# Kernel tuning notes

Hardware: AMD Instinct MI355X
Metric: run time of the kernel (lower is better)

## Reference

```python
import math
import jax, jax.numpy as jnp
import numpy as np
from jax.scipy.special import xlogy

B, N, INP, E = 128, 16, 1024, 512
MU, CLF, PLCY = 512, 512, 512
M = N - 1          # merges (full tree)
T = N + M          # total tree tokens
L = N + M - 1      # logits matrix side
NOISE_STD, MASK_VAL = 0.01, -9e20
SFTMX_EPS, STD_EPS = 1e-20, 1e-20


def _mlp3(x, w1, b1, w2, b2, w3, b3):
    h = jax.nn.relu(x @ w1 + b1)
    h = jax.nn.relu(h @ w2 + b2)
    return h @ w3 + b3


def _lin(key, fi, fo):
    lim = math.sqrt(6.0 / (fi + fo))  # xavier uniform
    return (jax.random.uniform(key, (fi, fo), minval=-lim, maxval=lim, dtype=jnp.float32),
            jnp.full((fo,), 0.001, dtype=jnp.float32))


def setup_inputs():
    key = jax.random.key(0)
    ks = jax.random.split(key, 16)
    inp = {"x": jax.random.normal(ks[0], (B, N, INP), dtype=jnp.float32)}
    inp["lift_w"], inp["lift_b"] = _lin(ks[1], INP, E)
    inp["unlift_w"], inp["unlift_b"] = _lin(ks[2], E, INP)
    inp["enc_w1"], inp["enc_b1"] = _lin(ks[3], 2 * E, MU)
    inp["enc_w2"], inp["enc_b2"] = _lin(ks[4], MU, MU)
    inp["enc_w3"], inp["enc_b3"] = _lin(ks[5], MU, E)
    inp["dec_w1"], inp["dec_b1"] = _lin(ks[6], E, MU)
    inp["dec_w2"], inp["dec_b2"] = _lin(ks[7], MU, MU)
    inp["dec_w3"], inp["dec_b3"] = _lin(ks[8], MU, 2 * E)
    inp["clf_w1"], inp["clf_b1"] = _lin(ks[9], E, CLF)
    inp["clf_w2"], inp["clf_b2"] = _lin(ks[10], CLF, CLF)
    inp["clf_w3"], inp["clf_b3"] = _lin(ks[11], CLF, 2)
    inp["pol_w1"], inp["pol_b1"] = _lin(ks[12], 2 * E, PLCY)
    inp["pol_w2"], inp["pol_b2"] = _lin(ks[13], PLCY, PLCY)
    inp["pol_w3"], inp["pol_b3"] = _lin(ks[14], PLCY, 1)
    return inp


def _forward(x, lift_w, lift_b, unlift_w, unlift_b,
             enc_w1, enc_b1, enc_w2, enc_b2, enc_w3, enc_b3,
             dec_w1, dec_b1, dec_w2, dec_b2, dec_w3, dec_b3,
             clf_w1, clf_b1, clf_w2, clf_b2, clf_w3, clf_b3,
             pol_w1, pol_b1, pol_w2, pol_b2, pol_w3, pol_b3):
    sg = jax.lax.stop_gradient
    enc = lambda z: _mlp3(z, enc_w1, enc_b1, enc_w2, enc_b2, enc_w3, enc_b3)
    dec = lambda z: _mlp3(z, dec_w1, dec_b1, dec_w2, dec_b2, dec_w3, dec_b3)
    clf = lambda z: _mlp3(z, clf_w1, clf_b1, clf_w2, clf_b2, clf_w3, clf_b3)
    pol = lambda z: _mlp3(z, pol_w1, pol_b1, pol_w2, pol_b2, pol_w3, pol_b3)
    base = jax.random.key(42)
    b_idx = jnp.arange(B)

    # lift + noise
    u = x @ lift_w + lift_b
    u = u + NOISE_STD * jax.random.normal(jax.random.fold_in(base, 7), u.shape, u.dtype)

    logits_mtx = jnp.full((B, L, L), MASK_VAL, dtype=jnp.float32)
    # iter 0: score all ordered pairs (i,j), i != j, among input tokens (vectorized)
    ii, jj = np.where(~np.eye(N, dtype=bool))                 # P = N*(N-1) static pairs
    pair_x = jnp.concatenate([u[:, ii], u[:, jj]], axis=-1)   # [B,P,2E]
    logits_mtx = logits_mtx.at[:, ii, jj].set(pol(sg(pair_x))[..., 0])

    active = jnp.tile(jnp.arange(N, dtype=jnp.int32), (B, 1))
    step_losses = jnp.zeros(B, dtype=jnp.float32)
    entropies = jnp.zeros(B, dtype=jnp.float32)
    actions, log_probs, rewards = [], [], []

    for it in range(M):
        A = active.shape[1]  # = N - it (active-token count at entry)
        if it > 0:
            nt = N + it - 1                      # newest merged token (last in active)
            act = active[:, :-1]                 # [B, A-1] older active tokens
            u_act = u[b_idx[:, None], act]       # [B, A-1, E]
            u_nt = jnp.broadcast_to(u[:, nt][:, None, :], u_act.shape)
            lg_f = pol(sg(jnp.concatenate([u_nt, u_act], -1)))[..., 0]
            lg_b = pol(sg(jnp.concatenate([u_act, u_nt], -1)))[..., 0]
            logits_mtx = logits_mtx.at[b_idx[:, None], nt, act].set(lg_f)
            logits_mtx = logits_mtx.at[b_idx[:, None], act, nt].set(lg_b)

        flat = logits_mtx.reshape(B, L * L)      # temp == 1 for learned policy
        p = jax.nn.softmax(flat, axis=1)
        P2 = L * L
        p_adj = (p + SFTMX_EPS) / (1.0 + P2 * SFTMX_EPS)
        val_norm = SFTMX_EPS / (1.0 + P2 * SFTMX_EPS)
        opt_norm = A * (A - 1)
        nopt = P2 - opt_norm
        entrop = -(jnp.sum(xlogy(p_adj, p_adj), axis=1)
                   - nopt * (val_norm * math.log(val_norm))) / math.log(opt_norm)
        entropies = entropies + entrop

        # multinomial sample over flattened (masked) logits matrix
        sflat = jax.random.categorical(jax.random.fold_in(base, 100 + it), flat)
        s0, s1 = sflat // L, sflat % L
        sample = jnp.stack([s0, s1], axis=1)     # [B,2]
        actions.append(sample)
        log_probs.append(jnp.log(p[b_idx, sflat]))

        # mask out rows/cols of the merged tokens
        logits_mtx = logits_mtx.at[b_idx[:, None], sample, :].set(MASK_VAL)
        logits_mtx = logits_mtx.at[b_idx[:, None], :, sample].set(MASK_VAL)

        # remove the two sampled tokens from the active set (order-preserving)
        keep = (active != s0[:, None].astype(active.dtype)) & (active != s1[:, None].astype(active.dtype))
        order = jnp.argsort((~keep).astype(jnp.int32), axis=1, stable=True)
        active = jnp.take_along_axis(active, order[:, :A - 2], axis=1)

        pair = jnp.concatenate([u[b_idx, s0], u[b_idx, s1]], axis=1)  # [B,2E]
        true_s = sg(pair)
        pred_s = dec(enc(true_s))
        osl = jnp.sum((pred_s - true_s) ** 2, axis=1) / (2 * E)
        step_losses = step_losses + osl
        rewards.append(-sg(osl))

        # merge: encode pair (grad flows into u here) + noise, append to tree
        mg = enc(pair)
        mg = mg + NOISE_STD * jax.random.normal(jax.random.fold_in(base, 1000 + it), mg.shape, mg.dtype)
        u = jnp.concatenate([u, mg[:, None, :]], axis=1)
        active = jnp.concatenate([active, jnp.full((B, 1), N + it, dtype=active.dtype)], axis=1)

    actions = jnp.stack(actions, axis=1)    # [B,M,2]
    log_probs = jnp.stack(log_probs, axis=1)
    rewards = jnp.stack(rewards, axis=1)

    # top-down decode
    d = jnp.zeros_like(u)
    d = d.at[b_idx[:, None], active].set(u[b_idx[:, None], active])  # seed remaining active (root)
    clf_rows = []
    for it in range(M):
        tok = T - 1 - it
        mgd = d[:, tok]
        unmg = dec(mgd).reshape(B, 2, E)
        d = d.at[b_idx[:, None], actions[:, M - 1 - it]].set(unmg)
        clf_rows.append(clf(sg(mgd)))
    clf_pred = jnp.concatenate(
        [jnp.stack(clf_rows, axis=1), clf(sg(d[:, :N]))[:, ::-1, :]], axis=1)  # [B,M+N,2]
    clf_lbl = jnp.tile(jnp.concatenate(
        [jnp.ones(M, dtype=jnp.int32), jnp.zeros(N, dtype=jnp.int32)]), (B, 1))

    step_losses = step_losses / M
    entropies = entropies / M
    mvg = rewards.reshape(-1)  # B*M <= mvg_adv_sz, so moving buffer == current rewards
    rew_n = (rewards - mvg.mean()) / (jnp.std(mvg, ddof=1) + STD_EPS)
    reinf = jnp.sum(log_probs * rew_n, axis=1)
    recon = d[:, :N] @ unlift_w + unlift_b
    return recon, u, d, step_losses, entropies, clf_pred, clf_lbl, reinf


def reference(x, lift_w, lift_b, unlift_w, unlift_b,
              enc_w1, enc_b1, enc_w2, enc_b2, enc_w3, enc_b3,
              dec_w1, dec_b1, dec_w2, dec_b2, dec_w3, dec_b3,
              clf_w1, clf_b1, clf_w2, clf_b2, clf_w3, clf_b3,
              pol_w1, pol_b1, pol_w2, pol_b2, pol_w3, pol_b3):
    return _forward(x, lift_w, lift_b, unlift_w, unlift_b,
                    enc_w1, enc_b1, enc_w2, enc_b2, enc_w3, enc_b3,
                    dec_w1, dec_b1, dec_w2, dec_b2, dec_w3, dec_b3,
                    clf_w1, clf_b1, clf_w2, clf_b2, clf_w3, clf_b3,
                    pol_w1, pol_b1, pol_w2, pol_b2, pol_w3, pol_b3)
```

## Files before the change

kernel.cpp:

```cpp
#include <hip/hip_runtime.h>
#include <cstdint>
#include <cmath>

#define MASKV -9.0e20f

__host__ __device__ inline void tf2x32(uint32_t k0, uint32_t k1, uint32_t& x0, uint32_t& x1){
  uint32_t ks2 = k0 ^ k1 ^ 0x1BD11BDAu;
  x0 += k0; x1 += k1;
#define TFR(r) { x0 += x1; x1 = (x1<<(r))|(x1>>(32-(r))); x1 ^= x0; }
  TFR(13) TFR(15) TFR(26) TFR(6)
  x0 += k1;  x1 += ks2 + 1u;
  TFR(17) TFR(29) TFR(16) TFR(24)
  x0 += ks2; x1 += k0 + 2u;
  TFR(13) TFR(15) TFR(26) TFR(6)
  x0 += k0;  x1 += k1 + 3u;
  TFR(17) TFR(29) TFR(16) TFR(24)
  x0 += k1;  x1 += ks2 + 4u;
  TFR(13) TFR(15) TFR(26) TFR(6)
  x0 += ks2; x1 += k0 + 5u;
#undef TFR
}

__device__ inline uint32_t rbits32(uint32_t k0, uint32_t k1, uint32_t idx){
  uint32_t x0 = 0u, x1 = idx;
  tf2x32(k0, k1, x0, x1);
  return x0 ^ x1;
}

__device__ inline float u01_from_bits(uint32_t bits){
  union { uint32_t u; float f; } c;
  c.u = (bits >> 9) | 0x3f800000u;
  return c.f - 1.0f;
}

__device__ inline float erfinv_f(float x){
  float w = -log1pf(-x*x);
  float p;
  if (w < 5.0f){
    w -= 2.5f;
    p = 2.81022636e-08f;
    p = fmaf(p, w, 3.43273939e-07f);
    p = fmaf(p, w, -3.5233877e-06f);
    p = fmaf(p, w, -4.39150654e-06f);
    p = fmaf(p, w, 0.00021858087f);
    p = fmaf(p, w, -0.00125372503f);
    p = fmaf(p, w, -0.00417768164f);
    p = fmaf(p, w, 0.246640727f);
    p = fmaf(p, w, 1.50140941f);
  } else {
    w = sqrtf(w) - 3.0f;
    p = -0.000200214257f;
    p = fmaf(p, w, 0.000100950558f);
    p = fmaf(p, w, 0.00134934322f);
    p = fmaf(p, w, -0.00367342844f);
    p = fmaf(p, w, 0.00573950773f);
    p = fmaf(p, w, -0.0076224613f);
    p = fmaf(p, w, 0.00943887047f);
    p = fmaf(p, w, 1.00167406f);
    p = fmaf(p, w, 2.83297682f);
  }
  return p * x;
}

__device__ inline float jax_normal(uint32_t k0, uint32_t k1, uint32_t idx){
  float f = u01_from_bits(rbits32(k0, k1, idx));
  float v = fmaf(f, 2.0f, -0.99999994f);
  v = fmaxf(v, -0.99999994f);
  return 1.41421356f * erfinv_f(v);
}

__device__ inline float jax_gumbel(uint32_t k0, uint32_t k1, uint32_t idx){
  float f = u01_from_bits(rbits32(k0, k1, idx));
  f = f + 1.17549435e-38f;
  f = fmaxf(f, 1.17549435e-38f);
  return -logf(-logf(f));
}

template<int ACT>
__global__ __launch_bounds__(256) void gemm_k(
    const float* __restrict__ A, int lda,
    const long* __restrict__ atab, int anblk,
    const float* __restrict__ W, const float* __restrict__ bias,
    float* __restrict__ C, int K, int N,
    long c_base, int c_rdiv, long c_ostride, long c_istride)
{
  __shared__ float As[16][64];
  __shared__ float Ws[16][64];
  int tid = threadIdx.x;
  int c0 = blockIdx.x * 64;
  int r0 = blockIdx.y * 64;
  int lr = tid >> 2;
  int lk = (tid & 3) << 2;
  int wk = tid >> 4;
  int wc = (tid & 15) << 2;
  int tx = tid & 15;
  int ty = tid >> 4;
  long aoff0 = 0, aoff1 = 0;
  if (atab){
    const long* t = atab + (long)(r0 + lr) * anblk;
    aoff0 = t[0];
    if (anblk == 2) aoff1 = t[1];
  } else {
    aoff0 = (long)(r0 + lr) * lda;
  }
  float acc[4][4];
#pragma unroll
  for (int i = 0; i < 4; i++)
#pragma unroll
    for (int j = 0; j < 4; j++) acc[i][j] = 0.f;

  for (int k0 = 0; k0 < K; k0 += 16){
    int ka = k0 + lk;
    long ab = (atab && anblk == 2 && ka >= 512) ? (aoff1 + (ka - 512)) : (aoff0 + ka);
    float4 av = *(const float4*)(A + ab);
    As[lk + 0][lr] = av.x;
    As[lk + 1][lr] = av.y;
    As[lk + 2][lr] = av.z;
    As[lk + 3][lr] = av.w;
    float4 wv = *(const float4*)(W + (long)(k0 + wk) * N + (c0 + wc));
    *(float4*)&Ws[wk][wc] = wv;
    __syncthreads();
#pragma unroll
    for (int kk = 0; kk < 16; kk++){
      float4 a4 = *(const float4*)&As[kk][ty << 2];
      float4 w4 = *(const float4*)&Ws[kk][tx << 2];
      float aa[4] = {a4.x, a4.y, a4.z, a4.w};
      float ww[4] = {w4.x, w4.y, w4.z, w4.w};
#pragma unroll
      for (int i = 0; i < 4; i++)
#pragma unroll
        for (int j = 0; j < 4; j++)
          acc[i][j] = fmaf(aa[i], ww[j], acc[i][j]);
    }
    __syncthreads();
  }
  float4 bv = *(const float4*)(bias + c0 + (tx << 2));
  float bb[4] = {bv.x, bv.y, bv.z, bv.w};
#pragma unroll
  for (int i = 0; i < 4; i++){
    int r = r0 + (ty << 2) + i;
    long off = c_base + (long)(r / c_rdiv) * c_ostride + (long)(r % c_rdiv) * c_istride
               + c0 + (tx << 2);
    float4 v;
    float o0 = acc[i][0] + bb[0], o1 = acc[i][1] + bb[1];
    float o2 = acc[i][2] + bb[2], o3 = acc[i][3] + bb[3];
    if (ACT){ o0 = fmaxf(o0, 0.f); o1 = fmaxf(o1, 0.f); o2 = fmaxf(o2, 0.f); o3 = fmaxf(o3, 0.f); }
    v.x = o0; v.y = o1; v.z = o2; v.w = o3;
    *(float4*)(C + off) = v;
  }
}

__global__ __launch_bounds__(256) void gemm128f_k(
    const float* __restrict__ Y,
    const long* __restrict__ atab,
    const float* __restrict__ b1,
    const float* __restrict__ W2, const float* __restrict__ b2,
    const float* __restrict__ w3,
    const int* __restrict__ scat, float* __restrict__ logits)
{
  __shared__ float As[16][132];
  __shared__ float Ws[16][132];
  int tid = threadIdx.x;
  int c0 = blockIdx.x * 128;
  int r0 = blockIdx.y * 128;
  int tx = tid & 15, ty = tid >> 4;
  int rA0 = tid >> 2;
  int rA1 = rA0 + 64;
  int kq = (tid & 3) << 2;
  long a00 = atab[(long)(r0 + rA0) * 2];
  long a01 = atab[(long)(r0 + rA0) * 2 + 1];
  long a10 = atab[(long)(r0 + rA1) * 2];
  long a11 = atab[(long)(r0 + rA1) * 2 + 1];
  int wk0 = tid >> 5, wc0 = (tid & 31) << 2;
  float acc[8][8];
#pragma unroll
  for (int i = 0; i < 8; i++)
#pragma unroll
    for (int j = 0; j < 8; j++) acc[i][j] = 0.f;

  for (int k0 = 0; k0 < 512; k0 += 16){
    int ka = k0 + kq;
    float4 p0 = *(const float4*)(Y + a00 + ka);
    float4 q0 = *(const float4*)(Y + a01 + ka);
    float4 p1 = *(const float4*)(Y + a10 + ka);
    float4 q1 = *(const float4*)(Y + a11 + ka);
    float4 bb = *(const float4*)(b1 + ka);
    As[kq + 0][rA0] = fmaxf(p0.x + q0.x + bb.x, 0.f);
    As[kq + 1][rA0] = fmaxf(p0.y + q0.y + bb.y, 0.f);
    As[kq + 2][rA0] = fmaxf(p0.z + q0.z + bb.z, 0.f);
    As[kq + 3][rA0] = fmaxf(p0.w + q0.w + bb.w, 0.f);
    As[kq + 0][rA1] = fmaxf(p1.x + q1.x + bb.x, 0.f);
    As[kq + 1][rA1] = fmaxf(p1.y + q1.y + bb.y, 0.f);
    As[kq + 2][rA1] = fmaxf(p1.z + q1.z + bb.z, 0.f);
    As[kq + 3][rA1] = fmaxf(p1.w + q1.w + bb.w, 0.f);
    *(float4*)&Ws[wk0][wc0]     = *(const float4*)(W2 + (long)(k0 + wk0) * 512 + (c0 + wc0));
    *(float4*)&Ws[wk0 + 8][wc0] = *(const float4*)(W2 + (long)(k0 + wk0 + 8) * 512 + (c0 + wc0));
    __syncthreads();
#pragma unroll
    for (int kk = 0; kk < 16; kk++){
      float a0[8], w0[8];
      *(float4*)&a0[0] = *(const float4*)&As[kk][ty << 3];
      *(float4*)&a0[4] = *(const float4*)&As[kk][(ty << 3) + 4];
      *(float4*)&w0[0] = *(const float4*)&Ws[kk][tx << 3];
      *(float4*)&w0[4] = *(const float4*)&Ws[kk][(tx << 3) + 4];
#pragma unroll
      for (int i = 0; i < 8; i++)
#pragma unroll
        for (int j = 0; j < 8; j++)
          acc[i][j] = fmaf(a0[i], w0[j], acc[i][j]);
    }
    __syncthreads();
  }
  float bb[8], w3v[8];
  *(float4*)&bb[0] = *(const float4*)(b2 + c0 + (tx << 3));
  *(float4*)&bb[4] = *(const float4*)(b2 + c0 + (tx << 3) + 4);
  *(float4*)&w3v[0] = *(const float4*)(w3 + c0 + (tx << 3));
  *(float4*)&w3v[4] = *(const float4*)(w3 + c0 + (tx << 3) + 4);
#pragma unroll
  for (int i = 0; i < 8; i++){
    float p = 0.f;
#pragma unroll
    for (int j = 0; j < 8; j++)
      p = fmaf(fmaxf(acc[i][j] + bb[j], 0.f), w3v[j], p);
    for (int m = 1; m < 16; m <<= 1) p += __shfl_xor(p, m);
    if (tx == 0){
      int r = r0 + (ty << 3) + i;
      atomicAdd(logits + scat[r], p);
    }
  }
}

__global__ __launch_bounds__(256) void gemm64f_k(
    const float* __restrict__ Y,
    const long* __restrict__ atab,
    const float* __restrict__ b1,
    const float* __restrict__ W2, const float* __restrict__ b2,
    const float* __restrict__ w3,
    const int* __restrict__ scat, float* __restrict__ logits)
{
  __shared__ float As[16][64];
  __shared__ float Ws[16][64];
  int tid = threadIdx.x;
  int c0 = blockIdx.x * 64;
  int r0 = blockIdx.y * 64;
  int lr = tid >> 2;
  int lk = (tid & 3) << 2;
  int wk = tid >> 4;
  int wc = (tid & 15) << 2;
  int tx = tid & 15;
  int ty = tid >> 4;
  long a0 = atab[(long)(r0 + lr) * 2];
  long a1 = atab[(long)(r0 + lr) * 2 + 1];
  float acc[4][4];
#pragma unroll
  for (int i = 0; i < 4; i++)
#pragma unroll
    for (int j = 0; j < 4; j++) acc[i][j] = 0.f;

  for (int k0 = 0; k0 < 512; k0 += 16){
    int ka = k0 + lk;
    float4 p = *(const float4*)(Y + a0 + ka);
    float4 q = *(const float4*)(Y + a1 + ka);
    float4 bb = *(const float4*)(b1 + ka);
    As[lk + 0][lr] = fmaxf(p.x + q.x + bb.x, 0.f);
    As[lk + 1][lr] = fmaxf(p.y + q.y + bb.y, 0.f);
    As[lk + 2][lr] = fmaxf(p.z + q.z + bb.z, 0.f);
    As[lk + 3][lr] = fmaxf(p.w + q.w + bb.w, 0.f);
    *(float4*)&Ws[wk][wc] = *(const float4*)(W2 + (long)(k0 + wk) * 512 + (c0 + wc));
    __syncthreads();
#pragma unroll
    for (int kk = 0; kk < 16; kk++){
      float4 a4 = *(const float4*)&As[kk][ty << 2];
      float4 w4 = *(const float4*)&Ws[kk][tx << 2];
      float aa[4] = {a4.x, a4.y, a4.z, a4.w};
      float ww[4] = {w4.x, w4.y, w4.z, w4.w};
#pragma unroll
      for (int i = 0; i < 4; i++)
#pragma unroll
        for (int j = 0; j < 4; j++)
          acc[i][j] = fmaf(aa[i], ww[j], acc[i][j]);
    }
    __syncthreads();
  }
  float bb4[4], w34[4];
  *(float4*)&bb4[0] = *(const float4*)(b2 + c0 + (tx << 2));
  *(float4*)&w34[0] = *(const float4*)(w3 + c0 + (tx << 2));
#pragma unroll
  for (int i = 0; i < 4; i++){
    float p = 0.f;
#pragma unroll
    for (int j = 0; j < 4; j++)
      p = fmaf(fmaxf(acc[i][j] + bb4[j], 0.f), w34[j], p);
    for (int m = 1; m < 16; m <<= 1) p += __shfl_xor(p, m);
    if (tx == 0){
      int r = r0 + (ty << 2) + i;
      atomicAdd(logits + scat[r], p);
    }
  }
}

__global__ __launch_bounds__(256) void rowdot_k(
    const float* __restrict__ A, int lda, const long* __restrict__ atab,
    const float* __restrict__ W, const float* __restrict__ bias,
    int K, int N, float* __restrict__ out, const int* __restrict__ scat,
    long c_base, int c_rdiv, long c_ostride, long c_istride)
{
  int wid = threadIdx.x >> 6, lane = threadIdx.x & 63;
  int r = blockIdx.x * 4 + wid;
  const float* a = atab ? (A + atab[r]) : (A + (long)r * lda);
  float s0 = 0.f, s1 = 0.f;
  for (int k = lane; k < K; k += 64){
    float x = a[k];
    s0 = fmaf(x, W[k * N], s0);
    if (N == 2) s1 = fmaf(x, W[k * N + 1], s1);
  }
  for (int off = 32; off > 0; off >>= 1){
    s0 += __shfl_down(s0, off);
    s1 += __shfl_down(s1, off);
  }
  if (lane == 0){
    if (scat){
      out[scat[r]] = s0 + bias[0];
    } else {
      long o = c_base + (long)(r / c_rdiv) * c_ostride + (long)(r % c_rdiv) * c_istride;
      out[o] = s0 + bias[0];
      if (N == 2) out[o + 1] = s1 + bias[1];
    }
  }
}

__global__ __launch_bounds__(256) void pairmv_k(
    const float* __restrict__ u, const long* __restrict__ tab_pair,
    const float* __restrict__ W, const float* __restrict__ bias,
    float* __restrict__ dst)
{
  __shared__ float s[1024];
  int b = blockIdx.y, tid = threadIdx.x;
  int c = blockIdx.x * 256 + tid;
  long t0 = tab_pair[b * 2], t1 = tab_pair[b * 2 + 1];
  s[tid]       = u[t0 + tid];
  s[tid + 256] = u[t0 + tid + 256];
  s[tid + 512] = u[t1 + tid];
  s[tid + 768] = u[t1 + tid + 256];
  __syncthreads();
  float a0 = 0.f, a1 = 0.f, a2 = 0.f, a3 = 0.f;
#pragma unroll 8
  for (int k = 0; k < 1024; k += 4){
    a0 = fmaf(s[k],     W[(long)k * 512 + c],       a0);
    a1 = fmaf(s[k + 1], W[(long)(k + 1) * 512 + c], a1);
    a2 = fmaf(s[k + 2], W[(long)(k + 2) * 512 + c], a2);
    a3 = fmaf(s[k + 3], W[(long)(k + 3) * 512 + c], a3);
  }
  float v = ((a0 + a1) + (a2 + a3)) + bias[c];
  dst[(long)b * 512 + c] = fmaxf(v, 0.f);
}

__global__ __launch_bounds__(256) void mvrelu_k(
    const float* __restrict__ src, long sstride,
    const float* __restrict__ W, const float* __restrict__ bias,
    float* __restrict__ dst)
{
  __shared__ float s[512];
  int b = blockIdx.y, tid = threadIdx.x;
  int c = blockIdx.x * 256 + tid;
  const float* sr = src + (long)b * sstride;
  s[tid] = sr[tid];
  s[tid + 256] = sr[tid + 256];
  __syncthreads();
  float a0 = 0.f, a1 = 0.f, a2 = 0.f, a3 = 0.f;
#pragma unroll 8
  for (int k = 0; k < 512; k += 4){
    a0 = fmaf(s[k],     W[(long)k * 512 + c],       a0);
    a1 = fmaf(s[k + 1], W[(long)(k + 1) * 512 + c], a1);
    a2 = fmaf(s[k + 2], W[(long)(k + 2) * 512 + c], a2);
    a3 = fmaf(s[k + 3], W[(long)(k + 3) * 512 + c], a3);
  }
  float v = ((a0 + a1) + (a2 + a3)) + bias[c];
  dst[(long)b * 512 + c] = fmaxf(v, 0.f);
}

__global__ __launch_bounds__(256) void lay3z_k(
    const float* __restrict__ src,
    const float* __restrict__ W, const float* __restrict__ bias,
    float* __restrict__ z_all, float* __restrict__ u,
    int it, uint32_t k0, uint32_t k1)
{
  __shared__ float s[512];
  int b = blockIdx.y, tid = threadIdx.x;
  int c = blockIdx.x * 256 + tid;
  const float* sr = src + (long)b * 512;
  s[tid] = sr[tid];
  s[tid + 256] = sr[tid + 256];
  __syncthreads();
  float a0 = 0.f, a1 = 0.f, a2 = 0.f, a3 = 0.f;
#pragma unroll 8
  for (int k = 0; k < 512; k += 4){
    a0 = fmaf(s[k],     W[(long)k * 512 + c],       a0);
    a1 = fmaf(s[k + 1], W[(long)(k + 1) * 512 + c], a1);
    a2 = fmaf(s[k + 2], W[(long)(k + 2) * 512 + c], a2);
    a3 = fmaf(s[k + 3], W[(long)(k + 3) * 512 + c], a3);
  }
  float v = ((a0 + a1) + (a2 + a3)) + bias[c];
  z_all[(long)it * 65536 + (long)b * 512 + c] = v;
  float nv = jax_normal(k0, k1, (uint32_t)(b * 512 + c));
  u[((long)(b * 31 + 16 + it)) * 512 + c] = v + 0.01f * nv;
}

__global__ __launch_bounds__(256) void yrow_k(
    const float* __restrict__ u, const float* __restrict__ W1cat,
    float* __restrict__ Y, int it)
{
  __shared__ float s[512];
  int b = blockIdx.y, tid = threadIdx.x;
  int c = blockIdx.x * 256 + tid;
  const float* sr = u + ((long)(b * 31 + 16 + it)) * 512;
  s[tid] = sr[tid];
  s[tid + 256] = sr[tid + 256];
  __syncthreads();
  float a0 = 0.f, a1 = 0.f, a2 = 0.f, a3 = 0.f;
#pragma unroll 8
  for (int k = 0; k < 512; k += 4){
    a0 = fmaf(s[k],     W1cat[(long)k * 1024 + c],       a0);
    a1 = fmaf(s[k + 1], W1cat[(long)(k + 1) * 1024 + c], a1);
    a2 = fmaf(s[k + 2], W1cat[(long)(k + 2) * 1024 + c], a2);
    a3 = fmaf(s[k + 3], W1cat[(long)(k + 3) * 1024 + c], a3);
  }
  Y[((long)(b * 31 + 16 + it)) * 1024 + c] = (a0 + a1) + (a2 + a3);
}

__global__ __launch_bounds__(256) void rev3_k(
    const float* __restrict__ src,
    const float* __restrict__ W, const float* __restrict__ bias,
    float* __restrict__ dmat, const int* __restrict__ actions, int it)
{
  __shared__ float s[512];
  int b = blockIdx.y, tid = threadIdx.x;
  int p = blockIdx.x * 256 + tid;
  const float* sr = src + (long)b * 512;
  s[tid] = sr[tid];
  s[tid + 256] = sr[tid + 256];
  __syncthreads();
  float a0 = 0.f, a1 = 0.f, a2 = 0.f, a3 = 0.f;
#pragma unroll 8
  for (int k = 0; k < 512; k += 4){
    a0 = fmaf(s[k],     W[(long)k * 1024 + p],       a0);
    a1 = fmaf(s[k + 1], W[(long)(k + 1) * 1024 + p], a1);
    a2 = fmaf(s[k + 2], W[(long)(k + 2) * 1024 + p], a2);
    a3 = fmaf(s[k + 3], W[(long)(k + 3) * 1024 + p], a3);
  }
  float v = ((a0 + a1) + (a2 + a3)) + bias[p];
  int fit = 14 - it;
  int s0 = actions[(b * 15 + fit) * 2];
  int s1 = actions[(b * 15 + fit) * 2 + 1];
  int node = (p < 512) ? s0 : s1;
  int ee = p & 511;
  dmat[((long)(b * 31 + node)) * 512 + ee] = v;
}

__global__ __launch_bounds__(256) void oslb_k(
    const float* __restrict__ pred, const float* __restrict__ u,
    const int* __restrict__ actions, float* __restrict__ sl, float* __restrict__ rew)
{
  int r = blockIdx.x, tid = threadIdx.x;
  int it = r >> 7, b = r & 127;
  int s0 = actions[(b * 15 + it) * 2];
  int s1 = actions[(b * 15 + it) * 2 + 1];
  const float* t0 = u + ((long)(b * 31 + s0)) * 512;
  const float* t1 = u + ((long)(b * 31 + s1)) * 512;
  const float* p = pred + (long)r * 1024;
  float s = 0.f;
  for (int k = tid; k < 512; k += 256){
    float d0 = p[k] - t0[k];       s = fmaf(d0, d0, s);
    float d1 = p[k + 512] - t1[k]; s = fmaf(d1, d1, s);
  }
  __shared__ float red[256];
  red[tid] = s; __syncthreads();
  for (int st = 128; st > 0; st >>= 1){ if (tid < st) red[tid] += red[tid + st]; __syncthreads(); }
  if (tid == 0){
    float osl = red[0] / 1024.0f;
    atomicAdd(sl + b, osl);
    rew[b * 15 + it] = -osl;
  }
}

__global__ __launch_bounds__(256) void init_k(float* __restrict__ dmat, float* __restrict__ lbl,
    float* __restrict__ logits, float* __restrict__ sl, float* __restrict__ ent,
    int* __restrict__ active, float* __restrict__ zb,
    float* __restrict__ W1cat, const float* __restrict__ pol_w1, const float* __restrict__ pol_b3,
    long* __restrict__ tab_init, int* __restrict__ scat_init, long* __restrict__ tab_tok16,
    long* __restrict__ tab_mgd)
{
  long i = (long)blockIdx.x * 256 + threadIdx.x;
  if (i < 2031616L) dmat[i] = 0.f;
  if (i < 524288L){
    int k = (int)(i >> 10), n = (int)(i & 1023);
    W1cat[i] = (n < 512) ? pol_w1[(long)k * 512 + n] : pol_w1[(long)(k + 512) * 512 + (n - 512)];
  }
  if (i < 115200L){
    int rem = (int)(i % 900);
    int rr = rem / 30, cc = rem % 30;
    logits[i] = (rr < 16 && cc < 16 && rr != cc) ? pol_b3[0] : MASKV;
  }
  if (i < 30720L){
    int r = (int)i;
    int pk = r >> 7, b = r & 127;
    int ii2 = pk / 15, jr = pk % 15;
    int jj2 = jr + (jr >= ii2 ? 1 : 0);
    tab_init[r * 2]     = ((long)(b * 31 + ii2)) * 1024;
    tab_init[r * 2 + 1] = ((long)(b * 31 + jj2)) * 1024 + 512;
    scat_init[r] = b * 900 + ii2 * 30 + jj2;
  }
  if (i < 3968L)  lbl[i] = ((i % 31) < 15) ? 1.0f : 0.0f;
  if (i < 2048L){
    active[i] = (int)(i & 15);
    tab_tok16[i] = ((long)((i >> 4) * 31 + (i & 15))) * 512;
  }
  if (i < 1920L){
    int it = (int)(i >> 7), b = (int)(i & 127);
    tab_mgd[i] = ((long)(b * 31 + 30 - it)) * 512;
  }
  if (i < 1024L)  zb[i] = 0.f;
  if (i < 128L){ sl[i] = 0.f; ent[i] = 0.f; }
}

__global__ __launch_bounds__(256) void noise_u_k(float* __restrict__ u, uint32_t k0, uint32_t k1){
  uint32_t e = blockIdx.x * 256u + threadIdx.x;
  uint32_t b = e >> 13, rem = e & 8191u, n = rem >> 9, ee = rem & 511u;
  float nr = jax_normal(k0, k1, e);
  long off = ((long)(b * 31u + n)) * 512 + ee;
  u[off] += 0.01f * nr;
}

__global__ __launch_bounds__(256) void build_d_k(float* __restrict__ dmat, const float* __restrict__ u){
  int e = blockIdx.x * 256 + threadIdx.x;
  int b = e >> 9, ee = e & 511;
  long off = ((long)(b * 31 + 30)) * 512 + ee;
  dmat[off] = u[off];
}

__global__ __launch_bounds__(256) void sample_k(float* __restrict__ logits, int* __restrict__ active,
    int* __restrict__ actions, float* __restrict__ lp, float* __restrict__ ent,
    int it, int A, uint32_t k0, uint32_t k1, float log_opt,
    long* __restrict__ tab_loop, int* __restrict__ scat_loop, long* __restrict__ tab_pair,
    const float* __restrict__ pol_b3)
{
  int b = blockIdx.x, tid = threadIdx.x;
  float* Lg = logits + (long)b * 900;
  __shared__ float red[256];
  __shared__ int redi[256];
  __shared__ int ss0, ss1;

  float v = -3.4e38f;
  for (int j = tid; j < 900; j += 256) v = fmaxf(v, Lg[j]);
  red[tid] = v; __syncthreads();
  for (int s = 128; s > 0; s >>= 1){ if (tid < s) red[tid] = fmaxf(red[tid], red[tid + s]); __syncthreads(); }
  float m = red[0]; __syncthreads();

  float acc = 0.f;
  for (int j = tid; j < 900; j += 256) acc += expf(Lg[j] - m);
  red[tid] = acc; __syncthreads();
  for (int s = 128; s > 0; s >>= 1){ if (tid < s) red[tid] += red[tid + s]; __syncthreads(); }
  float ssum = red[0]; __syncthreads();

  float es = 0.f;
  for (int j = tid; j < 900; j += 256){
    float l = Lg[j];
    if (l > MASKV){
      float p = expf(l - m) / ssum;
      float pa = p + 1e-20f;
      es += pa * logf(pa);
    }
  }
  red[tid] = es; __syncthreads();
  for (int s = 128; s > 0; s >>= 1){ if (tid < s) red[tid] += red[tid + s]; __syncthreads(); }
  if (tid == 0) ent[b] += -(red[0]) / log_opt;
  __syncthreads();

  float bv = -3.4e38f; int bi = 0;
  for (int j = tid; j < 900; j += 256){
    float g = jax_gumbel(k0, k1, (uint32_t)(b * 900 + j));
    float val = Lg[j] + g;
    if (val > bv){ bv = val; bi = j; }
  }
  red[tid] = bv; redi[tid] = bi; __syncthreads();
  for (int s = 128; s > 0; s >>= 1){
    if (tid < s){
      float o = red[tid + s]; int oi = redi[tid + s];
      if (o > red[tid] || (o == red[tid] && oi < redi[tid])){ red[tid] = o; redi[tid] = oi; }
    }
    __syncthreads();
  }
  if (tid == 0){
    int sf = redi[0];
    int s0 = sf / 30, s1 = sf % 30;
    ss0 = s0; ss1 = s1;
    actions[(b * 15 + it) * 2] = s0;
    actions[(b * 15 + it) * 2 + 1] = s1;
    lp[b * 15 + it] = Lg[sf] - m - logf(ssum);
    tab_pair[b * 2]     = ((long)(b * 31 + s0)) * 512;
    tab_pair[b * 2 + 1] = ((long)(b * 31 + s1)) * 512;
  }
  __syncthreads();
  int s0 = ss0, s1 = ss1;
  if (tid < 30){
    Lg[s0 * 30 + tid] = MASKV;
    Lg[s1 * 30 + tid] = MASKV;
    Lg[tid * 30 + s0] = MASKV;
    Lg[tid * 30 + s1] = MASKV;
  }
  if (tid == 0){
    float b3v = pol_b3[0];
    int buf[16]; int c = 0;
    for (int k = 0; k < A; k++){
      int a = active[b * 16 + k];
      if (a != s0 && a != s1) buf[c++] = a;
    }
    int nt2 = 16 + it;
    buf[c++] = nt2;
    for (int k = 0; k < c; k++) active[b * 16 + k] = buf[k];
    int na2 = c - 1;
    for (int j = 0; j < na2; j++){
      int q = buf[j];
      int r1 = j * 128 + b;
      tab_loop[r1 * 2]     = ((long)(b * 31 + nt2)) * 1024;
      tab_loop[r1 * 2 + 1] = ((long)(b * 31 + q)) * 1024 + 512;
      int sc1 = b * 900 + nt2 * 30 + q;
      scat_loop[r1] = sc1;
      logits[sc1] = b3v;
      int r2 = (na2 + j) * 128 + b;
      tab_loop[r2 * 2]     = ((long)(b * 31 + q)) * 1024;
      tab_loop[r2 * 2 + 1] = ((long)(b * 31 + nt2)) * 1024 + 512;
      int sc2 = b * 900 + q * 30 + nt2;
      scat_loop[r2] = sc2;
      logits[sc2] = b3v;
    }
  }
}

__global__ __launch_bounds__(256) void finalize_k(const float* __restrict__ rew,
    const float* __restrict__ lp, const float* __restrict__ sl, const float* __restrict__ ent,
    float* __restrict__ out_sl, float* __restrict__ out_ent, float* __restrict__ out_reinf)
{
  __shared__ float red[256];
  int tid = threadIdx.x;
  float s = 0.f;
  for (int i = tid; i < 1920; i += 256) s += rew[i];
  red[tid] = s; __syncthreads();
  for (int st = 128; st > 0; st >>= 1){ if (tid < st) red[tid] += red[tid + st]; __syncthreads(); }
  float mean = red[0] / 1920.0f; __syncthreads();
  float v = 0.f;
  for (int i = tid; i < 1920; i += 256){ float x = rew[i] - mean; v = fmaf(x, x, v); }
  red[tid] = v; __syncthreads();
  for (int st = 128; st > 0; st >>= 1){ if (tid < st) red[tid] += red[tid + st]; __syncthreads(); }
  float denom = sqrtf(red[0] / 1919.0f) + 1e-20f;
  if (tid < 128){
    out_sl[tid] = sl[tid] / 15.0f;
    out_ent[tid] = ent[tid] / 15.0f;
    float r = 0.f;
    for (int k = 0; k < 15; k++){
      float rn = (rew[tid * 15 + k] - mean) / denom;
      r = fmaf(lp[tid * 15 + k], rn, r);
    }
    out_reinf[tid] = r;
  }
}

extern "C" void kernel_launch(void* const* d_in, const int* in_sizes, int n_in,
                              void* d_out, int out_size, void* d_ws, size_t ws_size,
                              hipStream_t stream)
{
  const float* x        = (const float*)d_in[0];
  const float* lift_w   = (const float*)d_in[1];
  const float* lift_b   = (const float*)d_in[2];
  const float* unlift_w = (const float*)d_in[3];
  const float* unlift_b = (const float*)d_in[4];
  const float* enc_w1   = (const float*)d_in[5];
  const float* enc_b1   = (const float*)d_in[6];
  const float* enc_w2   = (const float*)d_in[7];
  const float* enc_b2   = (const float*)d_in[8];
  const float* enc_w3   = (const float*)d_in[9];
  const float* enc_b3   = (const float*)d_in[10];
  const float* dec_w1   = (const float*)d_in[11];
  const float* dec_b1   = (const float*)d_in[12];
  const float* dec_w2   = (const float*)d_in[13];
  const float* dec_b2   = (const float*)d_in[14];
  const float* dec_w3   = (const float*)d_in[15];
  const float* dec_b3   = (const float*)d_in[16];
  const float* clf_w1   = (const float*)d_in[17];
  const float* clf_b1   = (const float*)d_in[18];
  const float* clf_w2   = (const float*)d_in[19];
  const float* clf_b2   = (const float*)d_in[20];
  const float* clf_w3   = (const float*)d_in[21];
  const float* clf_b3   = (const float*)d_in[22];
  const float* pol_w1   = (const float*)d_in[23];
  const float* pol_b1   = (const float*)d_in[24];
  const float* pol_w2   = (const float*)d_in[25];
  const float* pol_b2   = (const float*)d_in[26];
  const float* pol_w3   = (const float*)d_in[27];
  const float* pol_b3   = (const float*)d_in[28];

  float* out = (float*)d_out;
  const long U_OFF     = 2097152;
  const long D_OFF     = 4128768;
  const long SL_OFF    = 6160384;
  const long ENT_OFF   = 6160512;
  const long CLF_OFF   = 6160640;
  const long LBL_OFF   = 6168576;
  const long REINF_OFF = 6172544;
  float* recon = out;
  float* u     = out + U_OFF;
  float* dmat  = out + D_OFF;

  char* wsb = (char*)d_ws;
  size_t wo = 0;
  auto alloc = [&](size_t bytes) -> void* {
    void* p = (void*)(wsb + wo);
    wo = (wo + bytes + 255) & ~(size_t)255;
    return p;
  };
  float* logits    = (float*)alloc(115200 * 4);
  float* Y         = (float*)alloc((size_t)3968 * 1024 * 4);
  float* pbuf      = Y;
  float* W1cat     = (float*)alloc((size_t)524288 * 4);
  float* zb        = (float*)alloc(1024 * 4);
  float* h1        = (float*)alloc((size_t)2048 * 512 * 4);
  float* h2        = (float*)alloc((size_t)2048 * 512 * 4);
  float* z_all     = (float*)alloc((size_t)15 * 65536 * 4);
  float* sl        = (float*)alloc(128 * 4);
  float* ent       = (float*)alloc(128 * 4);
  float* lp        = (float*)alloc(1920 * 4);
  float* rew       = (float*)alloc(1920 * 4);
  int*   active    = (int*)alloc(2048 * 4);
  int*   actions   = (int*)alloc(3840 * 4);
  long*  tab_init  = (long*)alloc((size_t)30720 * 2 * 8);
  int*   scat_init = (int*)alloc(30720 * 4);
  long*  tab_loop  = (long*)alloc((size_t)3584 * 2 * 8);
  int*   scat_loop = (int*)alloc(3584 * 4);
  long*  tab_pair  = (long*)alloc(256 * 8);
  long*  tab_tok16 = (long*)alloc(2048 * 8);
  long*  tab_mgd   = (long*)alloc(1920 * 8);
  (void)ws_size; (void)in_sizes; (void)n_in; (void)out_size;

  uint32_t k7a, k7b, ck0[15], ck1[15], mk0[15], mk1[15];
  { uint32_t a = 0, b = 7; tf2x32(0u, 42u, a, b); k7a = a; k7b = b; }
  for (int it = 0; it < 15; it++){
    { uint32_t a = 0, b = (uint32_t)(100 + it); tf2x32(0u, 42u, a, b); ck0[it] = a; ck1[it] = b; }
    { uint32_t a = 0, b = (uint32_t)(1000 + it); tf2x32(0u, 42u, a, b); mk0[it] = a; mk1[it] = b; }
  }

  auto gemm = [&](int act, const float* A, int lda, const long* atab, int anblk,
                  const float* W, const float* bs, float* C, int rows, int K, int Nn,
                  long cb, int crd, long cos, long cis){
    dim3 g(Nn / 64, rows / 64);
    if (act) gemm_k<1><<<g, 256, 0, stream>>>(A, lda, atab, anblk, W, bs, C, K, Nn, cb, crd, cos, cis);
    else     gemm_k<0><<<g, 256, 0, stream>>>(A, lda, atab, anblk, W, bs, C, K, Nn, cb, crd, cos, cis);
  };

  init_k<<<7936, 256, 0, stream>>>(dmat, out + LBL_OFF, logits, sl, ent, active, zb,
                                   W1cat, pol_w1, pol_b3, tab_init, scat_init, tab_tok16,
                                   tab_mgd);

  gemm(0, x, 1024, nullptr, 0, lift_w, lift_b, u, 2048, 1024, 512, 0, 16, 15872, 512);
  noise_u_k<<<4096, 256, 0, stream>>>(u, k7a, k7b);

  gemm(0, u, 0, tab_tok16, 1, W1cat, zb, Y, 2048, 512, 1024, 0, 16, 31744, 1024);

  { dim3 g(4, 240);
    gemm128f_k<<<g, 256, 0, stream>>>(Y, tab_init, pol_b1, pol_w2, pol_b2, pol_w3,
                                      scat_init, logits); }

  for (int it = 0; it < 15; it++){
    int A = 16 - it;
    if (it > 0){
      int rows = 256 * (15 - it);
      dim3 g(8, rows / 64);
      gemm64f_k<<<g, 256, 0, stream>>>(Y, tab_loop, pol_b1, pol_w2, pol_b2, pol_w3,
                                       scat_loop, logits);
    }
    float log_opt = (float)log((double)(A * (A - 1)));
    sample_k<<<128, 256, 0, stream>>>(logits, active, actions, lp, ent, it, A,
                                      ck0[it], ck1[it], log_opt,
                                      tab_loop, scat_loop, tab_pair, pol_b3);
    { dim3 g(2, 128);
      pairmv_k<<<g, 256, 0, stream>>>(u, tab_pair, enc_w1, enc_b1, h1); }
    { dim3 g(2, 128);
      mvrelu_k<<<g, 256, 0, stream>>>(h1, 512, enc_w2, enc_b2, h2); }
    { dim3 g(2, 128);
      lay3z_k<<<g, 256, 0, stream>>>(h2, enc_w3, enc_b3, z_all, u, it, mk0[it], mk1[it]); }
    if (it < 14){
      dim3 g(4, 128);
      yrow_k<<<g, 256, 0, stream>>>(u, W1cat, Y, it);
    }
  }

  gemm(1, z_all, 512, nullptr, 0, dec_w1, dec_b1, h1, 1920, 512, 512, 0, 1, 512, 0);
  gemm(1, h1, 512, nullptr, 0, dec_w2, dec_b2, h2, 1920, 512, 512, 0, 1, 512, 0);
  gemm(0, h2, 512, nullptr, 0, dec_w3, dec_b3, pbuf, 1920, 512, 1024, 0, 1, 1024, 0);
  oslb_k<<<1920, 256, 0, stream>>>(pbuf, u, actions, sl, rew);

  build_d_k<<<256, 256, 0, stream>>>(dmat, u);

  for (int it = 0; it < 15; it++){
    int tok = 30 - it;
    { dim3 g(2, 128);
      mvrelu_k<<<g, 256, 0, stream>>>(dmat + (long)tok * 512, 15872, dec_w1, dec_b1, h1); }
    { dim3 g(2, 128);
      mvrelu_k<<<g, 256, 0, stream>>>(h1, 512, dec_w2, dec_b2, h2); }
    { dim3 g(4, 128);
      rev3_k<<<g, 256, 0, stream>>>(h2, dec_w3, dec_b3, dmat, actions, it); }
  }

  gemm(1, dmat, 0, tab_mgd, 1, clf_w1, clf_b1, h1, 1920, 512, 512, 0, 1, 512, 0);
  gemm(1, h1, 512, nullptr, 0, clf_w2, clf_b2, h2, 1920, 512, 512, 0, 1, 512, 0);
  rowdot_k<<<480, 256, 0, stream>>>(h2, 512, nullptr, clf_w3, clf_b3, 512, 2,
                                    out, nullptr, CLF_OFF, 128, 2, 62);

  gemm(1, dmat, 0, tab_tok16, 1, clf_w1, clf_b1, h1, 2048, 512, 512, 0, 1, 512, 0);
  gemm(1, h1, 512, nullptr, 0, clf_w2, clf_b2, h2, 2048, 512, 512, 0, 1, 512, 0);
  rowdot_k<<<512, 256, 0, stream>>>(h2, 512, nullptr, clf_w3, clf_b3, 512, 2,
                                    out, nullptr, CLF_OFF + 60, 16, 62, -2);

  gemm(0, dmat, 0, tab_tok16, 1, unlift_w, unlift_b, recon, 2048, 512, 1024,
       0, 16, 16384, 1024);

  finalize_k<<<1, 256, 0, stream>>>(rew, lp, sl, ent,
                                    out + SL_OFF, out + ENT_OFF, out + REINF_OFF);
}
```

Measured before the change: 2.621 ms.

## Fuse encoder output with Y projection, batch classifier GEMMs, and remap gemm128 fragments

Four separate changes. The encoder's third layer and the per-step Y row projection now run in one 512-thread kernel, so each of the 15 iterations launches one kernel fewer and the new u row goes to the projection through shared memory. The two classifier MLP passes (merged rows and the 16 leaf tokens) are combined into one 3968-row gemm chain plus a single scatter-indexed rowdot, using a precomputed scatter table. Separately, gemm128f threads now read and write two 4-wide strided fragments instead of one 8-wide contiguous block, to ease LDS bank conflicts, and the full dmat zero-fill is dropped from init. The batching assumes tab_mgd and tab_tok16 sit next to each other in the workspace, and skipping the zero-fill assumes every needed dmat entry is written later.

```diff
diff --git a/kernel.cpp b/kernel.cpp
--- a/kernel.cpp
+++ b/kernel.cpp
@@ -199,10 +199,10 @@
 #pragma unroll
     for (int kk = 0; kk < 16; kk++){
       float a0[8], w0[8];
-      *(float4*)&a0[0] = *(const float4*)&As[kk][ty << 3];
-      *(float4*)&a0[4] = *(const float4*)&As[kk][(ty << 3) + 4];
-      *(float4*)&w0[0] = *(const float4*)&Ws[kk][tx << 3];
-      *(float4*)&w0[4] = *(const float4*)&Ws[kk][(tx << 3) + 4];
+      *(float4*)&a0[0] = *(const float4*)&As[kk][ty << 2];
+      *(float4*)&a0[4] = *(const float4*)&As[kk][(ty << 2) + 64];
+      *(float4*)&w0[0] = *(const float4*)&Ws[kk][tx << 2];
+      *(float4*)&w0[4] = *(const float4*)&Ws[kk][(tx << 2) + 64];
 #pragma unroll
       for (int i = 0; i < 8; i++)
 #pragma unroll
@@ -212,10 +212,10 @@
     __syncthreads();
   }
   float bb[8], w3v[8];
-  *(float4*)&bb[0] = *(const float4*)(b2 + c0 + (tx << 3));
-  *(float4*)&bb[4] = *(const float4*)(b2 + c0 + (tx << 3) + 4);
-  *(float4*)&w3v[0] = *(const float4*)(w3 + c0 + (tx << 3));
-  *(float4*)&w3v[4] = *(const float4*)(w3 + c0 + (tx << 3) + 4);
+  *(float4*)&bb[0]  = *(const float4*)(b2 + c0 + (tx << 2));
+  *(float4*)&bb[4]  = *(const float4*)(b2 + c0 + (tx << 2) + 64);
+  *(float4*)&w3v[0] = *(const float4*)(w3 + c0 + (tx << 2));
+  *(float4*)&w3v[4] = *(const float4*)(w3 + c0 + (tx << 2) + 64);
 #pragma unroll
   for (int i = 0; i < 8; i++){
     float p = 0.f;
@@ -224,8 +224,8 @@
       p = fmaf(fmaxf(acc[i][j] + bb[j], 0.f), w3v[j], p);
     for (int m = 1; m < 16; m <<= 1) p += __shfl_xor(p, m);
     if (tx == 0){
-      int r = r0 + (ty << 3) + i;
-      atomicAdd(logits + scat[r], p);
+      int rr = (i < 4) ? ((ty << 2) + i) : (64 + (ty << 2) + (i - 4));
+      atomicAdd(logits + scat[r0 + rr], p);
     }
   }
 }
@@ -299,33 +299,28 @@
   }
 }
 
-__global__ __launch_bounds__(256) void rowdot_k(
-    const float* __restrict__ A, int lda, const long* __restrict__ atab,
+__global__ __launch_bounds__(256) void rowdot2_k(
+    const float* __restrict__ A, int lda,
     const float* __restrict__ W, const float* __restrict__ bias,
-    int K, int N, float* __restrict__ out, const int* __restrict__ scat,
-    long c_base, int c_rdiv, long c_ostride, long c_istride)
+    int K, float* __restrict__ out, const int* __restrict__ scat)
 {
   int wid = threadIdx.x >> 6, lane = threadIdx.x & 63;
   int r = blockIdx.x * 4 + wid;
-  const float* a = atab ? (A + atab[r]) : (A + (long)r * lda);
+  const float* a = A + (long)r * lda;
   float s0 = 0.f, s1 = 0.f;
   for (int k = lane; k < K; k += 64){
     float x = a[k];
-    s0 = fmaf(x, W[k * N], s0);
-    if (N == 2) s1 = fmaf(x, W[k * N + 1], s1);
+    s0 = fmaf(x, W[k * 2], s0);
+    s1 = fmaf(x, W[k * 2 + 1], s1);
   }
   for (int off = 32; off > 0; off >>= 1){
     s0 += __shfl_down(s0, off);
     s1 += __shfl_down(s1, off);
   }
   if (lane == 0){
-    if (scat){
-      out[scat[r]] = s0 + bias[0];
-    } else {
-      long o = c_base + (long)(r / c_rdiv) * c_ostride + (long)(r % c_rdiv) * c_istride;
-      out[o] = s0 + bias[0];
-      if (N == 2) out[o + 1] = s1 + bias[1];
-    }
+    long o = scat[r];
+    out[o] = s0 + bias[0];
+    out[o + 1] = s1 + bias[1];
   }
 }
 
@@ -379,53 +374,46 @@
   dst[(long)b * 512 + c] = fmaxf(v, 0.f);
 }
 
-__global__ __launch_bounds__(256) void lay3z_k(
+__global__ __launch_bounds__(512) void lay3y_k(
     const float* __restrict__ src,
     const float* __restrict__ W, const float* __restrict__ bias,
-    float* __restrict__ z_all, float* __restrict__ u,
+    const float* __restrict__ W1cat,
+    float* __restrict__ z_all, float* __restrict__ u, float* __restrict__ Y,
     int it, uint32_t k0, uint32_t k1)
 {
   __shared__ float s[512];
-  int b = blockIdx.y, tid = threadIdx.x;
-  int c = blockIdx.x * 256 + tid;
-  const float* sr = src + (long)b * 512;
-  s[tid] = sr[tid];
-  s[tid + 256] = sr[tid + 256];
+  __shared__ float zu[512];
+  int b = blockIdx.x, tid = threadIdx.x;
+  s[tid] = src[(long)b * 512 + tid];
   __syncthreads();
   float a0 = 0.f, a1 = 0.f, a2 = 0.f, a3 = 0.f;
 #pragma unroll 8
   for (int k = 0; k < 512; k += 4){
-    a0 = fmaf(s[k],     W[(long)k * 512 + c],       a0);
-    a1 = fmaf(s[k + 1], W[(long)(k + 1) * 512 + c], a1);
-    a2 = fmaf(s[k + 2], W[(long)(k + 2) * 512 + c], a2);
-    a3 = fmaf(s[k + 3], W[(long)(k + 3) * 512 + c], a3);
-  }
-  float v = ((a0 + a1) + (a2 + a3)) + bias[c];
-  z_all[(long)it * 65536 + (long)b * 512 + c] = v;
-  float nv = jax_normal(k0, k1, (uint32_t)(b * 512 + c));
-  u[((long)(b * 31 + 16 + it)) * 512 + c] = v + 0.01f * nv;
-}
-
-__global__ __launch_bounds__(256) void yrow_k(
-    const float* __restrict__ u, const float* __restrict__ W1cat,
-    float* __restrict__ Y, int it)
-{
-  __shared__ float s[512];
-  int b = blockIdx.y, tid = threadIdx.x;
-  int c = blockIdx.x * 256 + tid;
-  const float* sr = u + ((long)(b * 31 + 16 + it)) * 512;
-  s[tid] = sr[tid];
-  s[tid + 256] = sr[tid + 256];
+    a0 = fmaf(s[k],     W[(long)k * 512 + tid],       a0);
+    a1 = fmaf(s[k + 1], W[(long)(k + 1) * 512 + tid], a1);
+    a2 = fmaf(s[k + 2], W[(long)(k + 2) * 512 + tid], a2);
+    a3 = fmaf(s[k + 3], W[(long)(k + 3) * 512 + tid], a3);
+  }
+  float z = ((a0 + a1) + (a2 + a3)) + bias[tid];
+  z_all[(long)it * 65536 + (long)b * 512 + tid] = z;
+  float uv = z + 0.01f * jax_normal(k0, k1, (uint32_t)(b * 512 + tid));
+  u[((long)(b * 31 + 16 + it)) * 512 + tid] = uv;
+  zu[tid] = uv;
   __syncthreads();
-  float a0 = 0.f, a1 = 0.f, a2 = 0.f, a3 = 0.f;
-#pragma unroll 8
-  for (int k = 0; k < 512; k += 4){
-    a0 = fmaf(s[k],     W1cat[(long)k * 1024 + c],       a0);
-    a1 = fmaf(s[k + 1], W1cat[(long)(k + 1) * 1024 + c], a1);
-    a2 = fmaf(s[k + 2], W1cat[(long)(k + 2) * 1024 + c], a2);
-    a3 = fmaf(s[k + 3], W1cat[(long)(k + 3) * 1024 + c], a3);
-  }
-  Y[((long)(b * 31 + 16 + it)) * 1024 + c] = (a0 + a1) + (a2 + a3);
+  if (it < 14){
+    float c0a = 0.f, c0b = 0.f, c1a = 0.f, c1b = 0.f;
+#pragma unroll 4
+    for (int k = 0; k < 512; k += 2){
+      float v0 = zu[k], v1 = zu[k + 1];
+      c0a = fmaf(v0, W1cat[(long)k * 1024 + tid],             c0a);
+      c1a = fmaf(v0, W1cat[(long)k * 1024 + tid + 512],       c1a);
+      c0b = fmaf(v1, W1cat[(long)(k + 1) * 1024 + tid],       c0b);
+      c1b = fmaf(v1, W1cat[(long)(k + 1) * 1024 + tid + 512], c1b);
+    }
+    long yo = ((long)(b * 31 + 16 + it)) * 1024;
+    Y[yo + tid] = c0a + c0b;
+    Y[yo + tid + 512] = c1a + c1b;
+  }
 }
 
 __global__ __launch_bounds__(256) void rev3_k(
@@ -483,15 +471,14 @@
   }
 }
 
-__global__ __launch_bounds__(256) void init_k(float* __restrict__ dmat, float* __restrict__ lbl,
+__global__ __launch_bounds__(256) void init_k(float* __restrict__ lbl,
     float* __restrict__ logits, float* __restrict__ sl, float* __restrict__ ent,
     int* __restrict__ active, float* __restrict__ zb,
     float* __restrict__ W1cat, const float* __restrict__ pol_w1, const float* __restrict__ pol_b3,
     long* __restrict__ tab_init, int* __restrict__ scat_init, long* __restrict__ tab_tok16,
-    long* __restrict__ tab_mgd)
+    long* __restrict__ tab_mgd, int* __restrict__ scat_clf, long clf_off)
 {
   long i = (long)blockIdx.x * 256 + threadIdx.x;
-  if (i < 2031616L) dmat[i] = 0.f;
   if (i < 524288L){
     int k = (int)(i >> 10), n = (int)(i & 1023);
     W1cat[i] = (n < 512) ? pol_w1[(long)k * 512 + n] : pol_w1[(long)(k + 512) * 512 + (n - 512)];
@@ -510,7 +497,16 @@
     tab_init[r * 2 + 1] = ((long)(b * 31 + jj2)) * 1024 + 512;
     scat_init[r] = b * 900 + ii2 * 30 + jj2;
   }
-  if (i < 3968L)  lbl[i] = ((i % 31) < 15) ? 1.0f : 0.0f;
+  if (i < 3968L){
+    lbl[i] = ((i % 31) < 15) ? 1.0f : 0.0f;
+    int r = (int)i;
+    if (r < 1920){
+      scat_clf[r] = (int)(clf_off + (long)(r & 127) * 62 + (r >> 7) * 2);
+    } else {
+      int rr = r - 1920;
+      scat_clf[r] = (int)(clf_off + (long)(rr >> 4) * 62 + 60 - ((rr & 15) << 1));
+    }
+  }
   if (i < 2048L){
     active[i] = (int)(i & 15);
     tab_tok16[i] = ((long)((i >> 4) * 31 + (i & 15))) * 512;
@@ -720,7 +716,9 @@
   };
   float* logits    = (float*)alloc(115200 * 4);
   float* Y         = (float*)alloc((size_t)3968 * 1024 * 4);
-  float* pbuf      = Y;
+  float* h1clf     = Y;
+  float* pbuf      = Y + 2031616;
+  float* h2clf     = Y + 2031616;
   float* W1cat     = (float*)alloc((size_t)524288 * 4);
   float* zb        = (float*)alloc(1024 * 4);
   float* h1        = (float*)alloc((size_t)2048 * 512 * 4);
@@ -737,8 +735,10 @@
   long*  tab_loop  = (long*)alloc((size_t)3584 * 2 * 8);
   int*   scat_loop = (int*)alloc(3584 * 4);
   long*  tab_pair  = (long*)alloc(256 * 8);
+  long*  tab_mgd   = (long*)alloc(1920 * 8);
   long*  tab_tok16 = (long*)alloc(2048 * 8);
-  long*  tab_mgd   = (long*)alloc(1920 * 8);
+  int*   scat_clf  = (int*)alloc(3968 * 4);
+  long*  tab_clf   = tab_mgd;
   (void)ws_size; (void)in_sizes; (void)n_in; (void)out_size;
 
   uint32_t k7a, k7b, ck0[15], ck1[15], mk0[15], mk1[15];
@@ -756,9 +756,9 @@
     else     gemm_k<0><<<g, 256, 0, stream>>>(A, lda, atab, anblk, W, bs, C, K, Nn, cb, crd, cos, cis);
   };
 
-  init_k<<<7936, 256, 0, stream>>>(dmat, out + LBL_OFF, logits, sl, ent, active, zb,
+  init_k<<<2048, 256, 0, stream>>>(out + LBL_OFF, logits, sl, ent, active, zb,
                                    W1cat, pol_w1, pol_b3, tab_init, scat_init, tab_tok16,
-                                   tab_mgd);
+                                   tab_mgd, scat_clf, CLF_OFF);
 
   gemm(0, x, 1024, nullptr, 0, lift_w, lift_b, u, 2048, 1024, 512, 0, 16, 15872, 512);
   noise_u_k<<<4096, 256, 0, stream>>>(u, k7a, k7b);
@@ -785,12 +785,8 @@
       pairmv_k<<<g, 256, 0, stream>>>(u, tab_pair, enc_w1, enc_b1, h1); }
     { dim3 g(2, 128);
       mvrelu_k<<<g, 256, 0, stream>>>(h1, 512, enc_w2, enc_b2, h2); }
-    { dim3 g(2, 128);
-      lay3z_k<<<g, 256, 0, stream>>>(h2, enc_w3, enc_b3, z_all, u, it, mk0[it], mk1[it]); }
-    if (it < 14){
-      dim3 g(4, 128);
-      yrow_k<<<g, 256, 0, stream>>>(u, W1cat, Y, it);
-    }
+    lay3y_k<<<128, 512, 0, stream>>>(h2, enc_w3, enc_b3, W1cat, z_all, u, Y,
+                                     it, mk0[it], mk1[it]);
   }
 
   gemm(1, z_all, 512, nullptr, 0, dec_w1, dec_b1, h1, 1920, 512, 512, 0, 1, 512, 0);
@@ -810,15 +806,9 @@
       rev3_k<<<g, 256, 0, stream>>>(h2, dec_w3, dec_b3, dmat, actions, it); }
   }
 
-  gemm(1, dmat, 0, tab_mgd, 1, clf_w1, clf_b1, h1, 1920, 512, 512, 0, 1, 512, 0);
-  gemm(1, h1, 512, nullptr, 0, clf_w2, clf_b2, h2, 1920, 512, 512, 0, 1, 512, 0);
-  rowdot_k<<<480, 256, 0, stream>>>(h2, 512, nullptr, clf_w3, clf_b3, 512, 2,
-                                    out, nullptr, CLF_OFF, 128, 2, 62);
-
-  gemm(1, dmat, 0, tab_tok16, 1, clf_w1, clf_b1, h1, 2048, 512, 512, 0, 1, 512, 0);
-  gemm(1, h1, 512, nullptr, 0, clf_w2, clf_b2, h2, 2048, 512, 512, 0, 1, 512, 0);
-  rowdot_k<<<512, 256, 0, stream>>>(h2, 512, nullptr, clf_w3, clf_b3, 512, 2,
-                                    out, nullptr, CLF_OFF + 60, 16, 62, -2);
+  gemm(1, dmat, 0, tab_clf, 1, clf_w1, clf_b1, h1clf, 3968, 512, 512, 0, 1, 512, 0);
+  gemm(1, h1clf, 512, nullptr, 0, clf_w2, clf_b2, h2clf, 3968, 512, 512, 0, 1, 512, 0);
+  rowdot2_k<<<992, 256, 0, stream>>>(h2clf, 512, clf_w3, clf_b3, 512, out, scat_clf);
 
   gemm(0, dmat, 0, tab_tok16, 1, unlift_w, unlift_b, recon, 2048, 512, 1024,
        0, 16, 16384, 1024);
```

Result: slower. 2.766 ms (+5.6%).
